# Performance work log

Hardware: AMD Instinct MI355X
Metric: run time of the kernel (lower is better)

## Reference

```python
import jax, jax.numpy as jnp
import numpy as np

D_MODEL = 128; D_STATE = 64; HEADDIM = 64; CHUNK = 64; EXPAND = 2
D_INNER = EXPAND * D_MODEL            # 256
NHEADS = D_INNER // HEADDIM           # 4
NGROUPS = 1; D_CONV = 4
D_XBC = D_INNER + 2 * NGROUPS * D_STATE          # 384
D_IN_PROJ = 2 * D_INNER + 2 * NGROUPS * D_STATE + NHEADS  # 644


def _segsum(x):
    # x: (..., L) -> (..., L, L) with [i, j] = sum_{j<k<=i} x_k, -inf above diag
    L = x.shape[-1]
    cs = jnp.cumsum(x, -1)
    d = cs[..., :, None] - cs[..., None, :]
    mask = jnp.tril(jnp.ones((L, L), bool))
    return jnp.where(mask, d, -jnp.inf)


def _mamba2(x, Wi, conv_w, conv_b, dt_bias, A_log, Dp, norm_w, Wo):
    b, l, _ = x.shape
    zxbcdt = x @ Wi.T                                    # (b,l,644)
    z = zxbcdt[..., :D_INNER]
    xBC = zxbcdt[..., D_INNER:D_INNER + D_XBC]
    dt = jax.nn.softplus(zxbcdt[..., D_INNER + D_XBC:] + dt_bias)  # (b,l,h)
    # causal depthwise conv1d, kernel 4
    xp = jnp.pad(xBC, ((0, 0), (D_CONV - 1, 0), (0, 0)))
    xBC = sum(xp[:, k:k + l, :] * conv_w[:, k] for k in range(D_CONV)) + conv_b
    xBC = jax.nn.silu(xBC)
    xs = xBC[..., :D_INNER].reshape(b, l, NHEADS, HEADDIM)
    Bm = xBC[..., D_INNER:D_INNER + D_STATE]             # (b,l,n) ngroups=1
    Cm = xBC[..., D_INNER + D_STATE:]                    # (b,l,n)
    A = -jnp.exp(A_log)                                  # (h,)
    # chunked SSD (ssd_minimal style)
    c = l // CHUNK
    X = xs.reshape(b, c, CHUNK, NHEADS, HEADDIM)
    dtc = dt.reshape(b, c, CHUNK, NHEADS)
    Bc = Bm.reshape(b, c, CHUNK, D_STATE)
    Cc = Cm.reshape(b, c, CHUNK, D_STATE)
    dA = jnp.transpose(dtc * A, (0, 3, 1, 2))            # (b,h,c,L)
    Acs = jnp.cumsum(dA, -1)
    Lm = jnp.exp(_segsum(dA))                            # (b,h,c,L,L)
    Xdt = X * dtc[..., None]                             # (b,c,L,h,p)
    Yd = jnp.einsum('bcln,bcsn,bhcls,bcshp->bclhp', Cc, Bc, Lm, Xdt)
    dec = jnp.exp(Acs[..., -1:] - Acs)                   # (b,h,c,L)
    st = jnp.einsum('bcln,bhcl,bclhp->bchpn', Bc, dec, Xdt)  # per-chunk states
    cd = jnp.exp(Acs[..., -1])                           # (b,h,c)
    def step(carry, inp):
        s, d = inp                                       # s:(b,h,p,n), d:(b,h)
        return carry * d[..., None, None] + s, carry
    init = jnp.zeros_like(st[:, 0])
    _, prev = jax.lax.scan(step, init, (jnp.moveaxis(st, 1, 0), jnp.moveaxis(cd, 2, 0)))
    prev = jnp.moveaxis(prev, 0, 1)                      # (b,c,h,p,n)
    Yo = jnp.einsum('bcln,bchpn,bhcl->bclhp', Cc, prev, jnp.exp(Acs))
    Y = (Yd + Yo).reshape(b, l, NHEADS, HEADDIM) + Dp[None, None, :, None] * xs
    # gated RMSNorm (norm_before_gate=False)
    y = Y.reshape(b, l, D_INNER) * jax.nn.silu(z)
    y = y * jax.lax.rsqrt(jnp.mean(y * y, -1, keepdims=True) + 1e-5) * norm_w
    return y @ Wo.T


def _init_params(key):
    ks = jax.random.split(key, 5)
    dt = jnp.exp(jax.random.uniform(ks[2], (NHEADS,)) * (np.log(0.1) - np.log(0.001)) + np.log(0.001))
    return {
        'Wi': jax.random.normal(ks[0], (D_IN_PROJ, D_MODEL), jnp.float32) * (D_MODEL ** -0.5),
        'conv_w': jax.random.normal(ks[1], (D_XBC, D_CONV), jnp.float32) * 0.3,
        'conv_b': jnp.zeros((D_XBC,), jnp.float32),
        'dt_bias': jnp.log(jnp.expm1(dt)),
        'A_log': jnp.log(jax.random.uniform(ks[3], (NHEADS,)) * 15.0 + 1.0),
        'D': jnp.ones((NHEADS,), jnp.float32),
        'norm_w': jnp.ones((D_INNER,), jnp.float32),
        'Wo': jax.random.normal(ks[4], (D_MODEL, D_INNER), jnp.float32) * (D_INNER ** -0.5),
    }


def setup_inputs() -> dict:
    key = jax.random.key(0)
    kx, kf, kb = jax.random.split(key, 3)
    inp = {'x': jax.random.normal(kx, (16, 2048, D_MODEL), jnp.float32)}
    for sfx, kk in (('_f', kf), ('_b', kb)):
        p = _init_params(kk)
        for name, v in p.items():
            inp[name + sfx] = v
    return inp


def reference(x, Wi_f, conv_w_f, conv_b_f, dt_bias_f, A_log_f, D_f, norm_w_f, Wo_f,
              Wi_b, conv_w_b, conv_b_b, dt_bias_b, A_log_b, D_b, norm_w_b, Wo_b):
    h_f = _mamba2(x, Wi_f, conv_w_f, conv_b_f, dt_bias_f, A_log_f, D_f, norm_w_f, Wo_f)
    h_b = jnp.flip(_mamba2(jnp.flip(x, 1), Wi_b, conv_w_b, conv_b_b, dt_bias_b, A_log_b, D_b, norm_w_b, Wo_b), 1)
    return h_f + h_b
```

## Files before the change

kernel.cpp:

```cpp
#include <hip/hip_runtime.h>
#include <hip/hip_bf16.h>
#include <cmath>

#define B_    16
#define L_    2048
#define T_    32768
#define DM_   128
#define DI_   256
#define DXBC_ 384
#define DS_   64
#define HD_   64
#define NH_   4
#define NC_   32

typedef __hip_bfloat16 bf16;
typedef __attribute__((ext_vector_type(8))) short short8;
typedef __attribute__((ext_vector_type(4))) float f32x4;

__device__ __forceinline__ float b2f(bf16 v) { return __bfloat162float(v); }
__device__ __forceinline__ bf16  f2b(float f) { return __float2bfloat16(f); }
__device__ __forceinline__ short f2bs(float f) { bf16 h = __float2bfloat16(f); return *reinterpret_cast<short*>(&h); }
__device__ __forceinline__ float bs2f(short s) { bf16 h = *reinterpret_cast<bf16*>(&s); return __bfloat162float(h); }
__device__ __forceinline__ float sigmoidf_(float x) { return 1.f / (1.f + expf(-x)); }
__device__ __forceinline__ float softplusf_(float x) { return (x > 20.f) ? x : log1pf(expf(x)); }
__device__ __forceinline__ float expneg_(float x) { return expf(fminf(x, 0.f)); }

struct __align__(8) S4 { short a, b, c, d; };

#define NWI 82432
#define NWO 32768

__global__ __launch_bounds__(256) void k_prep(
    const float* __restrict__ x,
    const float* __restrict__ WiF, const float* __restrict__ WiB,
    const float* __restrict__ WoF, const float* __restrict__ WoB,
    bf16* __restrict__ Xb, bf16* __restrict__ WiFb, bf16* __restrict__ WiBb,
    bf16* __restrict__ WoFb, bf16* __restrict__ WoBb)
{
    const int gid = blockIdx.x * 256 + threadIdx.x;
    const int stride = gridDim.x * 256;
    for (int i = gid; i < 1048576; i += stride) {
        float4 v = ((const float4*)x)[i];
        S4 s = { f2bs(v.x), f2bs(v.y), f2bs(v.z), f2bs(v.w) };
        ((S4*)Xb)[i] = s;
    }
    for (int i = gid; i < NWI / 4; i += stride) {
        float4 v = ((const float4*)WiF)[i];
        S4 s = { f2bs(v.x), f2bs(v.y), f2bs(v.z), f2bs(v.w) };
        ((S4*)WiFb)[i] = s;
        v = ((const float4*)WiB)[i];
        S4 t = { f2bs(v.x), f2bs(v.y), f2bs(v.z), f2bs(v.w) };
        ((S4*)WiBb)[i] = t;
    }
    for (int i = gid; i < NWO / 4; i += stride) {
        float4 v = ((const float4*)WoF)[i];
        S4 s = { f2bs(v.x), f2bs(v.y), f2bs(v.z), f2bs(v.w) };
        ((S4*)WoFb)[i] = s;
        v = ((const float4*)WoB)[i];
        S4 t = { f2bs(v.x), f2bs(v.y), f2bs(v.z), f2bs(v.w) };
        ((S4*)WoBb)[i] = t;
    }
}

__global__ __launch_bounds__(256) void k_inproj_mfma(
    const bf16* __restrict__ Xb, const bf16* __restrict__ WiFb, const bf16* __restrict__ WiBb,
    const float* __restrict__ cwF, const float* __restrict__ cbF,
    const float* __restrict__ cwB, const float* __restrict__ cbB,
    const float* __restrict__ dtbF, const float* __restrict__ dtbB,
    bf16* __restrict__ Z, bf16* __restrict__ XBC, float* __restrict__ DTV)
{
    const int tid  = threadIdx.x;
    const int wave = tid >> 6, lane = tid & 63;
    const int ln15 = lane & 15, q = lane >> 4;
    const int dir  = blockIdx.y;
    const bf16* Wi = dir ? WiBb : WiFb;
    const int t0 = blockIdx.x * 64;
    const int batch = t0 >> 11, l0 = t0 & (L_ - 1);
    const size_t rowbase = (size_t)dir * T_ + t0;

    __shared__ __align__(16) short xs[80][136];
    __shared__ __align__(16) short raws[80][80];

    for (int u = tid; u < 1280; u += 256) {
        int r = u >> 4, g = u & 15;
        int l = l0 - 16 + r;
        short8 v = {0, 0, 0, 0, 0, 0, 0, 0};
        if (l >= 0) {
            int sl = dir ? (L_ - 1 - l) : l;
            v = *(const short8*)(Xb + ((size_t)batch * L_ + sl) * DM_ + g * 8);
        }
        *(short8*)&xs[r][g * 8] = v;
    }
    __syncthreads();

#pragma unroll
    for (int zt = 0; zt < 4; ++zt) {
        const int c0 = zt * 64;
        short8 wf[4];
#pragma unroll
        for (int ks = 0; ks < 4; ++ks)
            wf[ks] = *(const short8*)(Wi + (size_t)(c0 + 16 * wave + ln15) * DM_ + ks * 32 + q * 8);
#pragma unroll
        for (int ct = 0; ct < 4; ++ct) {
            f32x4 acc = (f32x4){0.f, 0.f, 0.f, 0.f};
#pragma unroll
            for (int ks = 0; ks < 4; ++ks) {
                short8 xf = *(const short8*)&xs[16 + 16 * ct + ln15][ks * 32 + q * 8];
                acc = __builtin_amdgcn_mfma_f32_16x16x32_bf16(wf[ks], xf, acc, 0, 0, 0);
            }
            S4 s = { f2bs(acc[0]), f2bs(acc[1]), f2bs(acc[2]), f2bs(acc[3]) };
            *(S4*)(Z + (rowbase + 16 * ct + ln15) * DI_ + c0 + 16 * wave + 4 * q) = s;
        }
    }

    for (int nt = 4; nt < 10; ++nt) {
        const int c0 = nt * 64;
        short8 bf[4];
#pragma unroll
        for (int ks = 0; ks < 4; ++ks)
            bf[ks] = *(const short8*)(Wi + (size_t)(c0 + 16 * wave + ln15) * DM_ + ks * 32 + q * 8);
        f32x4 acc[5];
#pragma unroll
        for (int mt = 0; mt < 5; ++mt) acc[mt] = (f32x4){0.f, 0.f, 0.f, 0.f};
#pragma unroll
        for (int ks = 0; ks < 4; ++ks)
#pragma unroll
            for (int mt = 0; mt < 5; ++mt) {
                short8 afr = *(const short8*)&xs[16 * mt + ln15][ks * 32 + q * 8];
                acc[mt] = __builtin_amdgcn_mfma_f32_16x16x32_bf16(afr, bf[ks], acc[mt], 0, 0, 0);
            }
        __syncthreads();
#pragma unroll
        for (int mt = 0; mt < 5; ++mt)
#pragma unroll
            for (int rg = 0; rg < 4; ++rg)
                raws[16 * mt + 4 * q + rg][16 * wave + ln15] = f2bs(acc[mt][rg]);
        __syncthreads();

        const float* cw = dir ? cwB : cwF;
        const float* cb = dir ? cbB : cbF;
        for (int u = tid; u < 1024; u += 256) {
            int row = u >> 4, c4 = (u & 15) * 4;
            float s0[4];
            int ch0 = c0 - 256 + c4;
#pragma unroll
            for (int j = 0; j < 4; ++j) s0[j] = cb[ch0 + j];
#pragma unroll
            for (int k = 0; k < 4; ++k) {
                S4 rv = *(const S4*)&raws[13 + row + k][c4];
                short rr[4] = { rv.a, rv.b, rv.c, rv.d };
#pragma unroll
                for (int j = 0; j < 4; ++j) s0[j] += bs2f(rr[j]) * cw[(ch0 + j) * 4 + k];
            }
            short o[4];
#pragma unroll
            for (int j = 0; j < 4; ++j) { float s = s0[j]; s = s * sigmoidf_(s); o[j] = f2bs(s); }
            S4 s4 = { o[0], o[1], o[2], o[3] };
            *(S4*)(XBC + (rowbase + row) * DXBC_ + ch0) = s4;
        }
    }

    if (wave == 0) {
        short8 bf[4];
#pragma unroll
        for (int ks = 0; ks < 4; ++ks) {
            short8 v = {0, 0, 0, 0, 0, 0, 0, 0};
            if (ln15 < 4) v = *(const short8*)(Wi + (size_t)(640 + ln15) * DM_ + ks * 32 + q * 8);
            bf[ks] = v;
        }
        const float* dtb = dir ? dtbB : dtbF;
#pragma unroll
        for (int s = 0; s < 4; ++s) {
            f32x4 acc = (f32x4){0.f, 0.f, 0.f, 0.f};
#pragma unroll
            for (int ks = 0; ks < 4; ++ks) {
                short8 afr = *(const short8*)&xs[16 + 16 * s + ln15][ks * 32 + q * 8];
                acc = __builtin_amdgcn_mfma_f32_16x16x32_bf16(afr, bf[ks], acc, 0, 0, 0);
            }
            if (ln15 < 4) {
                float bias = dtb[ln15];
#pragma unroll
                for (int rg = 0; rg < 4; ++rg)
                    DTV[(rowbase + 16 * s + 4 * q + rg) * NH_ + ln15] = softplusf_(acc[rg] + bias);
            }
        }
    }
}

__global__ __launch_bounds__(256) void k_chunkdiag_mfma(
    const bf16* __restrict__ XBC, const float* __restrict__ DTV,
    const float* __restrict__ AlF, const float* __restrict__ AlB,
    const float* __restrict__ DpF, const float* __restrict__ DpB,
    bf16* __restrict__ Y, bf16* __restrict__ ST, float* __restrict__ CDb)
{
    const int tid = threadIdx.x;
    const int wave = tid >> 6, lane = tid & 63;
    const int ln15 = lane & 15, q = lane >> 4;
    const int c = blockIdx.x;
    const int b = blockIdx.y >> 2;
    const int h = blockIdx.y & 3;
    const int dir = blockIdx.z;
    const float Ah = -expf((dir ? AlB : AlF)[h]);
    const float Dh = (dir ? DpB : DpF)[h];
    const int t0 = b * L_ + c * 64;
    const size_t rowbase = (size_t)dir * T_ + t0;

    __shared__ __align__(16) short Bs[64][72];
    __shared__ __align__(16) short Cs[64][72];
    __shared__ __align__(16) short Xt[64][72];
    __shared__ __align__(16) short Bt[64][72];
    __shared__ float dts[64];
    __shared__ float Acs[64];
    __shared__ float decs[64];

    if (tid < 64) {
        int l = tid;
        float dt = DTV[(rowbase + l) * NH_ + h];
        dts[l] = dt;
        float s = dt * Ah;
#pragma unroll
        for (int off = 1; off < 64; off <<= 1) {
            float t2 = __shfl_up(s, off);
            if (l >= off) s += t2;
        }
        Acs[l] = s;
        float alast = __shfl(s, 63);
        decs[l] = expneg_(alast - s);
        if (l == 0) CDb[(((size_t)dir * B_ + b) * NH_ + h) * NC_ + c] = expneg_(alast);
    }
    __syncthreads();

    for (int u = tid; u < 512; u += 256) {
        int r = u >> 3, g = u & 7;
        size_t base = (rowbase + r) * DXBC_;
        *(short8*)&Bs[r][g * 8] = *(const short8*)(XBC + base + 256 + g * 8);
        *(short8*)&Cs[r][g * 8] = *(const short8*)(XBC + base + 320 + g * 8);
    }
    for (int u = tid; u < 4096; u += 256) {
        int l = u >> 6, p = u & 63;
        Xt[p][l] = f2bs(b2f(XBC[(rowbase + l) * DXBC_ + h * HD_ + p]) * dts[l]);
    }
    for (int u = tid; u < 4096; u += 256) {
        int l = u >> 6, n = u & 63;
        Bt[n][l] = f2bs(b2f(XBC[(rowbase + l) * DXBC_ + 256 + n]) * decs[l]);
    }
    __syncthreads();

    f32x4 a1[4];
#pragma unroll
    for (int ct = 0; ct < 4; ++ct) a1[ct] = (f32x4){0.f, 0.f, 0.f, 0.f};
#pragma unroll
    for (int ks = 0; ks < 2; ++ks) {
        short8 afr = *(const short8*)&Cs[16 * wave + ln15][ks * 32 + q * 8];
#pragma unroll
        for (int ct = 0; ct < 4; ++ct) {
            short8 bfr = *(const short8*)&Bs[16 * ct + ln15][ks * 32 + q * 8];
            a1[ct] = __builtin_amdgcn_mfma_f32_16x16x32_bf16(afr, bfr, a1[ct], 0, 0, 0);
        }
    }
#pragma unroll
    for (int ct = 0; ct < 4; ++ct)
#pragma unroll
        for (int rg = 0; rg < 4; ++rg) {
            int l = 16 * wave + 4 * q + rg, s = 16 * ct + ln15;
            float m = (s <= l) ? a1[ct][rg] * expneg_(Acs[l] - Acs[s]) : 0.f;
            Cs[l][s] = f2bs(m);
        }
    f32x4 a2[4];
#pragma unroll
    for (int ct = 0; ct < 4; ++ct) a2[ct] = (f32x4){0.f, 0.f, 0.f, 0.f};
#pragma unroll
    for (int ks = 0; ks < 2; ++ks) {
        short8 afr = *(const short8*)&Cs[16 * wave + ln15][ks * 32 + q * 8];
#pragma unroll
        for (int ct = 0; ct < 4; ++ct) {
            short8 bfr = *(const short8*)&Xt[16 * ct + ln15][ks * 32 + q * 8];
            a2[ct] = __builtin_amdgcn_mfma_f32_16x16x32_bf16(afr, bfr, a2[ct], 0, 0, 0);
        }
    }
#pragma unroll
    for (int ct = 0; ct < 4; ++ct)
#pragma unroll
        for (int rg = 0; rg < 4; ++rg) {
            int l = 16 * wave + 4 * q + rg, p = 16 * ct + ln15;
            size_t tI = rowbase + l;
            float xraw = b2f(XBC[tI * DXBC_ + h * HD_ + p]);
            Y[tI * DI_ + h * HD_ + p] = f2b(a2[ct][rg] + Dh * xraw);
        }
    f32x4 a3[4];
#pragma unroll
    for (int ct = 0; ct < 4; ++ct) a3[ct] = (f32x4){0.f, 0.f, 0.f, 0.f};
#pragma unroll
    for (int ks = 0; ks < 2; ++ks) {
        short8 afr = *(const short8*)&Xt[16 * wave + ln15][ks * 32 + q * 8];
#pragma unroll
        for (int ct = 0; ct < 4; ++ct) {
            short8 bfr = *(const short8*)&Bt[16 * ct + ln15][ks * 32 + q * 8];
            a3[ct] = __builtin_amdgcn_mfma_f32_16x16x32_bf16(afr, bfr, a3[ct], 0, 0, 0);
        }
    }
    size_t sb = ((((size_t)dir * B_ + b) * NC_ + c) * NH_ + h) * 4096;
#pragma unroll
    for (int ct = 0; ct < 4; ++ct)
#pragma unroll
        for (int rg = 0; rg < 4; ++rg) {
            int p = 16 * wave + 4 * q + rg, n = 16 * ct + ln15;
            ST[sb + p * 64 + n] = f2b(a3[ct][rg]);
        }
}

__global__ __launch_bounds__(256) void k_scan(bf16* __restrict__ ST, const float* __restrict__ CDb)
{
    const int tid = threadIdx.x;
    const int dir = blockIdx.y;
    const int bx = blockIdx.x;
    const int b = bx >> 4, h = (bx >> 2) & 3, qt = bx & 3;
    const size_t cdbase = (((size_t)dir * B_ + b) * NH_ + h) * NC_;
    float carry[4] = {0.f, 0.f, 0.f, 0.f};
    for (int c = 0; c < NC_; ++c) {
        const float cd = CDb[cdbase + c];
        size_t base = ((((size_t)dir * B_ + b) * NC_ + c) * NH_ + h) * 4096 + qt * 1024 + tid;
#pragma unroll
        for (int q = 0; q < 4; ++q) {
            float v = b2f(ST[base + q * 256]);
            ST[base + q * 256] = f2b(carry[q]);
            carry[q] = carry[q] * cd + v;
        }
    }
}

__global__ __launch_bounds__(256) void k_offdiag_fused(
    const bf16* __restrict__ XBC, const float* __restrict__ DTV,
    const float* __restrict__ AlF, const float* __restrict__ AlB,
    const bf16* __restrict__ ST, const bf16* __restrict__ Z,
    const float* __restrict__ nwF, const float* __restrict__ nwB,
    bf16* __restrict__ Y)
{
    const int tid = threadIdx.x;
    const int wave = tid >> 6, lane = tid & 63;
    const int ln15 = lane & 15, q = lane >> 4;
    const int c = blockIdx.x, b = blockIdx.y, dir = blockIdx.z;
    const float* Al = dir ? AlB : AlF;
    const int t0 = b * L_ + c * 64;
    const size_t rowbase = (size_t)dir * T_ + t0;

    __shared__ __align__(16) short Cs[64][72];
    __shared__ __align__(16) short Ps[64][72];
    __shared__ __align__(16) short Yz[64][264];
    __shared__ float eA[NH_][64];

    {
        float A = -expf(Al[wave]);
        float s = DTV[(rowbase + lane) * NH_ + wave] * A;
#pragma unroll
        for (int off = 1; off < 64; off <<= 1) {
            float t2 = __shfl_up(s, off);
            if (lane >= off) s += t2;
        }
        eA[wave][lane] = expneg_(s);
    }
    for (int u = tid; u < 512; u += 256) {
        int r = u >> 3, g = u & 7;
        *(short8*)&Cs[r][g * 8] = *(const short8*)(XBC + (rowbase + r) * DXBC_ + 320 + g * 8);
    }
    for (int u = lane; u < 512; u += 64) {
        int r = 16 * wave + (u >> 5), g = u & 31;
        *(short8*)&Yz[r][g * 8] = *(const short8*)(Y + (rowbase + r) * DI_ + g * 8);
    }

    for (int h = 0; h < NH_; ++h) {
        __syncthreads();
        size_t sb = ((((size_t)dir * B_ + b) * NC_ + c) * NH_ + h) * 4096;
        for (int u = tid; u < 512; u += 256) {
            int r = u >> 3, g = u & 7;
            *(short8*)&Ps[r][g * 8] = *(const short8*)(ST + sb + r * 64 + g * 8);
        }
        __syncthreads();

        f32x4 acc[4];
#pragma unroll
        for (int ct = 0; ct < 4; ++ct) acc[ct] = (f32x4){0.f, 0.f, 0.f, 0.f};
#pragma unroll
        for (int ks = 0; ks < 2; ++ks) {
            short8 afr = *(const short8*)&Cs[16 * wave + ln15][ks * 32 + q * 8];
#pragma unroll
            for (int ct = 0; ct < 4; ++ct) {
                short8 bfr = *(const short8*)&Ps[16 * ct + ln15][ks * 32 + q * 8];
                acc[ct] = __builtin_amdgcn_mfma_f32_16x16x32_bf16(afr, bfr, acc[ct], 0, 0, 0);
            }
        }
#pragma unroll
        for (int ct = 0; ct < 4; ++ct)
#pragma unroll
            for (int rg = 0; rg < 4; ++rg) {
                int l = 16 * wave + 4 * q + rg, p = 16 * ct + ln15;
                float yv = bs2f(Yz[l][h * 64 + p]) + acc[ct][rg] * eA[h][l];
                Yz[l][h * 64 + p] = f2bs(yv);
            }
    }

    const float* nw = dir ? nwB : nwF;
    float nwv[4];
#pragma unroll
    for (int j = 0; j < 4; ++j) nwv[j] = nw[lane * 4 + j];
    for (int rr = 0; rr < 16; ++rr) {
        int row = 16 * wave + rr;
        S4 zv4 = *(const S4*)(Z + (rowbase + row) * DI_ + lane * 4);
        short zr[4] = { zv4.a, zv4.b, zv4.c, zv4.d };
        float v[4]; float ss = 0.f;
#pragma unroll
        for (int j = 0; j < 4; ++j) {
            float yv = bs2f(Yz[row][lane * 4 + j]);
            float zf = bs2f(zr[j]);
            v[j] = yv * zf * sigmoidf_(zf);
            ss += v[j] * v[j];
        }
#pragma unroll
        for (int off = 1; off < 64; off <<= 1) ss += __shfl_xor(ss, off);
        float rn = rsqrtf(ss * (1.f / 256.f) + 1e-5f);
        S4 o = { f2bs(v[0] * rn * nwv[0]), f2bs(v[1] * rn * nwv[1]),
                 f2bs(v[2] * rn * nwv[2]), f2bs(v[3] * rn * nwv[3]) };
        *(S4*)(Y + (rowbase + row) * DI_ + lane * 4) = o;
    }
}

__global__ __launch_bounds__(256) void k_outproj_mfma(
    const bf16* __restrict__ Y, const bf16* __restrict__ WoFb, const bf16* __restrict__ WoBb,
    float* __restrict__ out)
{
    const int tid = threadIdx.x;
    const int wave = tid >> 6, lane = tid & 63;
    const int ln15 = lane & 15, q = lane >> 4;
    const int t0 = blockIdx.x * 64;
    const int batch = t0 >> 11;
    const int l0 = t0 & (L_ - 1);

    __shared__ __align__(16) short ys[64][264];

    f32x4 acc[8];
#pragma unroll
    for (int ct = 0; ct < 8; ++ct) acc[ct] = (f32x4){0.f, 0.f, 0.f, 0.f};

    for (int dir = 0; dir < 2; ++dir) {
        const bf16* Wo = dir ? WoBb : WoFb;
        __syncthreads();
        for (int u = tid; u < 2048; u += 256) {
            int r = u >> 5, g = u & 31;
            int tsrc = dir ? (batch * L_ + (L_ - 1 - (l0 + r))) : (t0 + r);
            *(short8*)&ys[r][g * 8] =
                *(const short8*)(Y + ((size_t)dir * T_ + tsrc) * DI_ + g * 8);
        }
        __syncthreads();
#pragma unroll
        for (int kk = 0; kk < 8; ++kk) {
            short8 afr = *(const short8*)&ys[16 * wave + ln15][kk * 32 + q * 8];
#pragma unroll
            for (int ct = 0; ct < 8; ++ct) {
                short8 bfr = *(const short8*)(Wo + (size_t)(16 * ct + ln15) * DI_ + kk * 32 + q * 8);
                acc[ct] = __builtin_amdgcn_mfma_f32_16x16x32_bf16(afr, bfr, acc[ct], 0, 0, 0);
            }
        }
    }
#pragma unroll
    for (int ct = 0; ct < 8; ++ct)
#pragma unroll
        for (int rg = 0; rg < 4; ++rg) {
            int row = 16 * wave + 4 * q + rg, col = 16 * ct + ln15;
            out[((size_t)(t0 + row)) * DM_ + col] = acc[ct][rg];
        }
}

extern "C" void kernel_launch(void* const* d_in, const int* in_sizes, int n_in,
                              void* d_out, int out_size, void* d_ws, size_t ws_size,
                              hipStream_t stream)
{
    const float* x    = (const float*)d_in[0];
    const float* WiF  = (const float*)d_in[1];
    const float* cwF  = (const float*)d_in[2];
    const float* cbF  = (const float*)d_in[3];
    const float* dtbF = (const float*)d_in[4];
    const float* AlF  = (const float*)d_in[5];
    const float* DpF  = (const float*)d_in[6];
    const float* nwF  = (const float*)d_in[7];
    const float* WoF  = (const float*)d_in[8];
    const float* WiB  = (const float*)d_in[9];
    const float* cwB  = (const float*)d_in[10];
    const float* cbB  = (const float*)d_in[11];
    const float* dtbB = (const float*)d_in[12];
    const float* AlB  = (const float*)d_in[13];
    const float* DpB  = (const float*)d_in[14];
    const float* nwB  = (const float*)d_in[15];
    const float* WoB  = (const float*)d_in[16];

    const size_t nZ   = (size_t)2 * T_ * DI_;
    const size_t nXBC = (size_t)2 * T_ * DXBC_;
    const size_t nY   = (size_t)2 * T_ * DI_;
    const size_t nST  = (size_t)2 * B_ * NC_ * NH_ * HD_ * DS_;
    const size_t nWb  = (size_t)2 * NWI + 2 * NWO;
    const size_t nDTV = (size_t)2 * T_ * NH_;
    const size_t nCD  = (size_t)2 * B_ * NH_ * NC_;
    const size_t need = (nZ + nXBC + nY + nST + nWb) * sizeof(bf16)
                      + (nDTV + nCD) * sizeof(float);
    if (ws_size < need) return;

    char* p = (char*)d_ws;
    bf16* Z    = (bf16*)p;            p += nZ * sizeof(bf16);
    bf16* XBC  = (bf16*)p;            p += nXBC * sizeof(bf16);
    bf16* Yb   = (bf16*)p;            p += nY * sizeof(bf16);
    bf16* ST   = (bf16*)p;            p += nST * sizeof(bf16);
    bf16* WiFb = (bf16*)p;            p += (size_t)NWI * sizeof(bf16);
    bf16* WiBb = (bf16*)p;            p += (size_t)NWI * sizeof(bf16);
    bf16* WoFb = (bf16*)p;            p += (size_t)NWO * sizeof(bf16);
    bf16* WoBb = (bf16*)p;            p += (size_t)NWO * sizeof(bf16);
    float* DTV = (float*)p;           p += nDTV * sizeof(float);
    float* CDb = (float*)p;
    bf16* Xb   = ST;

    k_prep<<<2048, 256, 0, stream>>>(x, WiF, WiB, WoF, WoB, Xb, WiFb, WiBb, WoFb, WoBb);
    k_inproj_mfma<<<dim3(512, 2), 256, 0, stream>>>(Xb, WiFb, WiBb, cwF, cbF, cwB, cbB,
                                                    dtbF, dtbB, Z, XBC, DTV);
    k_chunkdiag_mfma<<<dim3(NC_, B_ * NH_, 2), 256, 0, stream>>>(XBC, DTV, AlF, AlB, DpF, DpB,
                                                                 Yb, ST, CDb);
    k_scan<<<dim3(256, 2), 256, 0, stream>>>(ST, CDb);
    k_offdiag_fused<<<dim3(NC_, B_, 2), 256, 0, stream>>>(XBC, DTV, AlF, AlB, ST, Z,
                                                          nwF, nwB, Yb);
    k_outproj_mfma<<<dim3(512), 256, 0, stream>>>(Yb, WoFb, WoBb, (float*)d_out);
}
```

Measured before the change: 289.2 us.

## Use fast math intrinsics, hoist conv weights, reuse LDS X, retile outproj

Swaps expf/log1pf/division for fast __expf/__logf/rcp intrinsics. Hoists the conv weights and bias into registers outside the row loop in the in-projection kernel. Recovers the raw x for the D skip term from the LDS Xdt tile times the reciprocal of dt, instead of reloading it from global memory. Restructures the out-projection to 512 threads, staging Wo tiles in LDS over four K-steps and splitting the N dimension across waves. The fast intrinsics and reciprocal-dt reconstruction lose some precision, since Xt holds bf16 x*dt.

```diff
diff --git a/kernel.cpp b/kernel.cpp
--- a/kernel.cpp
+++ b/kernel.cpp
@@ -21,9 +21,10 @@
 __device__ __forceinline__ bf16  f2b(float f) { return __float2bfloat16(f); }
 __device__ __forceinline__ short f2bs(float f) { bf16 h = __float2bfloat16(f); return *reinterpret_cast<short*>(&h); }
 __device__ __forceinline__ float bs2f(short s) { bf16 h = *reinterpret_cast<bf16*>(&s); return __bfloat162float(h); }
-__device__ __forceinline__ float sigmoidf_(float x) { return 1.f / (1.f + expf(-x)); }
-__device__ __forceinline__ float softplusf_(float x) { return (x > 20.f) ? x : log1pf(expf(x)); }
-__device__ __forceinline__ float expneg_(float x) { return expf(fminf(x, 0.f)); }
+__device__ __forceinline__ float frcp_(float x) { return __builtin_amdgcn_rcpf(x); }
+__device__ __forceinline__ float sigmoidf_(float x) { return frcp_(1.f + __expf(-x)); }
+__device__ __forceinline__ float softplusf_(float x) { return (x > 20.f) ? x : __logf(1.f + __expf(x)); }
+__device__ __forceinline__ float expneg_(float x) { return __expf(fminf(x, 0.f)); }
 
 struct __align__(8) S4 { short a, b, c, d; };
 
@@ -113,6 +114,9 @@
         }
     }
 
+    const float* cw = dir ? cwB : cwF;
+    const float* cb = dir ? cbB : cbF;
+    const int c4 = (tid & 15) * 4;
     for (int nt = 4; nt < 10; ++nt) {
         const int c0 = nt * 64;
         short8 bf[4];
@@ -129,6 +133,14 @@
                 short8 afr = *(const short8*)&xs[16 * mt + ln15][ks * 32 + q * 8];
                 acc[mt] = __builtin_amdgcn_mfma_f32_16x16x32_bf16(afr, bf[ks], acc[mt], 0, 0, 0);
             }
+        const int ch0 = c0 - 256 + c4;
+        float cwr[4][4], cbr[4];
+#pragma unroll
+        for (int j = 0; j < 4; ++j) {
+            cbr[j] = cb[ch0 + j];
+#pragma unroll
+            for (int k = 0; k < 4; ++k) cwr[j][k] = cw[(ch0 + j) * 4 + k];
+        }
         __syncthreads();
 #pragma unroll
         for (int mt = 0; mt < 5; ++mt)
@@ -137,20 +149,18 @@
                 raws[16 * mt + 4 * q + rg][16 * wave + ln15] = f2bs(acc[mt][rg]);
         __syncthreads();
 
-        const float* cw = dir ? cwB : cwF;
-        const float* cb = dir ? cbB : cbF;
-        for (int u = tid; u < 1024; u += 256) {
-            int row = u >> 4, c4 = (u & 15) * 4;
+#pragma unroll
+        for (int it = 0; it < 4; ++it) {
+            int row = (tid >> 4) + 16 * it;
             float s0[4];
-            int ch0 = c0 - 256 + c4;
-#pragma unroll
-            for (int j = 0; j < 4; ++j) s0[j] = cb[ch0 + j];
+#pragma unroll
+            for (int j = 0; j < 4; ++j) s0[j] = cbr[j];
 #pragma unroll
             for (int k = 0; k < 4; ++k) {
                 S4 rv = *(const S4*)&raws[13 + row + k][c4];
                 short rr[4] = { rv.a, rv.b, rv.c, rv.d };
 #pragma unroll
-                for (int j = 0; j < 4; ++j) s0[j] += bs2f(rr[j]) * cw[(ch0 + j) * 4 + k];
+                for (int j = 0; j < 4; ++j) s0[j] += bs2f(rr[j]) * cwr[j][k];
             }
             short o[4];
 #pragma unroll
@@ -200,7 +210,7 @@
     const int b = blockIdx.y >> 2;
     const int h = blockIdx.y & 3;
     const int dir = blockIdx.z;
-    const float Ah = -expf((dir ? AlB : AlF)[h]);
+    const float Ah = -__expf((dir ? AlB : AlF)[h]);
     const float Dh = (dir ? DpB : DpF)[h];
     const int t0 = b * L_ + c * 64;
     const size_t rowbase = (size_t)dir * T_ + t0;
@@ -210,6 +220,7 @@
     __shared__ __align__(16) short Xt[64][72];
     __shared__ __align__(16) short Bt[64][72];
     __shared__ float dts[64];
+    __shared__ float rdts[64];
     __shared__ float Acs[64];
     __shared__ float decs[64];
 
@@ -217,6 +228,7 @@
         int l = tid;
         float dt = DTV[(rowbase + l) * NH_ + h];
         dts[l] = dt;
+        rdts[l] = frcp_(dt);
         float s = dt * Ah;
 #pragma unroll
         for (int off = 1; off < 64; off <<= 1) {
@@ -283,9 +295,8 @@
 #pragma unroll
         for (int rg = 0; rg < 4; ++rg) {
             int l = 16 * wave + 4 * q + rg, p = 16 * ct + ln15;
-            size_t tI = rowbase + l;
-            float xraw = b2f(XBC[tI * DXBC_ + h * HD_ + p]);
-            Y[tI * DI_ + h * HD_ + p] = f2b(a2[ct][rg] + Dh * xraw);
+            float xraw = bs2f(Xt[p][l]) * rdts[l];
+            Y[(rowbase + l) * DI_ + h * HD_ + p] = f2b(a2[ct][rg] + Dh * xraw);
         }
     f32x4 a3[4];
 #pragma unroll
@@ -350,7 +361,7 @@
     __shared__ float eA[NH_][64];
 
     {
-        float A = -expf(Al[wave]);
+        float A = -__expf(Al[wave]);
         float s = DTV[(rowbase + lane) * NH_ + wave] * A;
 #pragma unroll
         for (int off = 1; off < 64; off <<= 1) {
@@ -424,48 +435,58 @@
     }
 }
 
-__global__ __launch_bounds__(256) void k_outproj_mfma(
+__global__ __launch_bounds__(512) void k_outproj_mfma(
     const bf16* __restrict__ Y, const bf16* __restrict__ WoFb, const bf16* __restrict__ WoBb,
     float* __restrict__ out)
 {
     const int tid = threadIdx.x;
     const int wave = tid >> 6, lane = tid & 63;
     const int ln15 = lane & 15, q = lane >> 4;
+    const int mt = wave & 3, nh = wave >> 2;
     const int t0 = blockIdx.x * 64;
     const int batch = t0 >> 11;
     const int l0 = t0 & (L_ - 1);
 
-    __shared__ __align__(16) short ys[64][264];
-
-    f32x4 acc[8];
-#pragma unroll
-    for (int ct = 0; ct < 8; ++ct) acc[ct] = (f32x4){0.f, 0.f, 0.f, 0.f};
+    __shared__ __align__(16) short ys[64][72];
+    __shared__ __align__(16) short wsm[128][72];
+
+    f32x4 acc[4];
+#pragma unroll
+    for (int ct = 0; ct < 4; ++ct) acc[ct] = (f32x4){0.f, 0.f, 0.f, 0.f};
 
     for (int dir = 0; dir < 2; ++dir) {
         const bf16* Wo = dir ? WoBb : WoFb;
-        __syncthreads();
-        for (int u = tid; u < 2048; u += 256) {
-            int r = u >> 5, g = u & 31;
-            int tsrc = dir ? (batch * L_ + (L_ - 1 - (l0 + r))) : (t0 + r);
-            *(short8*)&ys[r][g * 8] =
-                *(const short8*)(Y + ((size_t)dir * T_ + tsrc) * DI_ + g * 8);
-        }
-        __syncthreads();
-#pragma unroll
-        for (int kk = 0; kk < 8; ++kk) {
-            short8 afr = *(const short8*)&ys[16 * wave + ln15][kk * 32 + q * 8];
-#pragma unroll
-            for (int ct = 0; ct < 8; ++ct) {
-                short8 bfr = *(const short8*)(Wo + (size_t)(16 * ct + ln15) * DI_ + kk * 32 + q * 8);
-                acc[ct] = __builtin_amdgcn_mfma_f32_16x16x32_bf16(afr, bfr, acc[ct], 0, 0, 0);
-            }
-        }
-    }
-#pragma unroll
-    for (int ct = 0; ct < 8; ++ct)
+        for (int kt = 0; kt < 4; ++kt) {
+            const int k0 = kt * 64;
+            __syncthreads();
+            {
+                int u = tid;
+                int r = u >> 3, g = u & 7;
+                int tsrc = dir ? (batch * L_ + (L_ - 1 - (l0 + r))) : (t0 + r);
+                *(short8*)&ys[r][g * 8] =
+                    *(const short8*)(Y + ((size_t)dir * T_ + tsrc) * DI_ + k0 + g * 8);
+            }
+            for (int u = tid; u < 1024; u += 512) {
+                int m = u >> 3, g = u & 7;
+                *(short8*)&wsm[m][g * 8] = *(const short8*)(Wo + (size_t)m * DI_ + k0 + g * 8);
+            }
+            __syncthreads();
+#pragma unroll
+            for (int ks = 0; ks < 2; ++ks) {
+                short8 afr = *(const short8*)&ys[16 * mt + ln15][ks * 32 + q * 8];
+#pragma unroll
+                for (int ct = 0; ct < 4; ++ct) {
+                    short8 bfr = *(const short8*)&wsm[16 * (4 * nh + ct) + ln15][ks * 32 + q * 8];
+                    acc[ct] = __builtin_amdgcn_mfma_f32_16x16x32_bf16(afr, bfr, acc[ct], 0, 0, 0);
+                }
+            }
+        }
+    }
+#pragma unroll
+    for (int ct = 0; ct < 4; ++ct)
 #pragma unroll
         for (int rg = 0; rg < 4; ++rg) {
-            int row = 16 * wave + 4 * q + rg, col = 16 * ct + ln15;
+            int row = 16 * mt + 4 * q + rg, col = 16 * (4 * nh + ct) + ln15;
             out[((size_t)(t0 + row)) * DM_ + col] = acc[ct][rg];
         }
 }
@@ -524,5 +545,5 @@
     k_scan<<<dim3(256, 2), 256, 0, stream>>>(ST, CDb);
     k_offdiag_fused<<<dim3(NC_, B_, 2), 256, 0, stream>>>(XBC, DTV, AlF, AlB, ST, Z,
                                                           nwF, nwB, Yb);
-    k_outproj_mfma<<<dim3(512), 256, 0, stream>>>(Yb, WoFb, WoBb, (float*)d_out);
-}
+    k_outproj_mfma<<<dim3(512), 512, 0, stream>>>(Yb, WoFb, WoBb, (float*)d_out);
+}
```

After: 242.7 us. 1.19x faster.
